# Kernel tuning notes

Measured on AMD Instinct MI355X. Metric: run time of the kernel, lower is better.

## Reference

```python
import jax, jax.numpy as jnp
import numpy as np

BITS = 4
MAXQ = (1 << BITS) - 1          # 15
ELEMS = 32 // BITS              # values packed per int32
GROUPSIZE = 128
M, K, N = 4096, 4096, 11008
G = K // GROUPSIZE              # 32 groups


def dequantize(qweight, scales, qzeros, g_idx):
    """Unpack GPTQ int4 weights -> fp16 [K, N], matching matmul_248_kernel."""
    K_ = g_idx.shape[0]
    N_ = scales.shape[1]
    k = jnp.arange(K_)
    # weight: value k,n packed in qweight[k // ELEMS, n] at bit offset (k % ELEMS)*BITS
    w = (qweight[k // ELEMS] >> ((k % ELEMS) * BITS)[:, None].astype(jnp.int32)) & MAXQ  # [K, N]
    # zeros: value g,n packed in qzeros[g, n // ELEMS] at bit offset (n % ELEMS)*BITS; kernel adds +1
    n = jnp.arange(N_)
    z = ((qzeros[:, n // ELEMS] >> ((n % ELEMS) * BITS)[None, :].astype(jnp.int32)) & MAXQ) + 1  # [G, N]
    gi = g_idx.astype(jnp.int32)
    # b = (b - zeros) * scales, per-group via g_idx row mapping
    W = scales[gi] * (w - z[gi]).astype(scales.dtype)  # fp16 [K, N]
    return W


def setup_inputs() -> dict:
    key = jax.random.key(0)
    k1, k2, k3, k4 = jax.random.split(key, 4)
    x = (jax.random.normal(k1, (M, K), dtype=jnp.float32) * 0.05).astype(jnp.float16)
    imin = jnp.iinfo(jnp.int32).min
    imax = jnp.iinfo(jnp.int32).max
    qweight = jax.random.randint(k2, (K // ELEMS, N), imin, imax, dtype=jnp.int32)
    qzeros = jax.random.randint(k3, (G, N // ELEMS), imin, imax, dtype=jnp.int32)
    scales = (jax.random.uniform(k4, (G, N), dtype=jnp.float32) * 0.009 + 0.001).astype(jnp.float16)
    g_idx = (jnp.arange(K, dtype=jnp.int32) // GROUPSIZE).astype(jnp.int32)
    return {"x": x, "qweight": qweight, "scales": scales, "qzeros": qzeros, "g_idx": g_idx}


def reference(x, qweight, scales, qzeros, g_idx):
    W = dequantize(qweight, scales, qzeros, g_idx)
    # fp16 inputs, fp32 accumulation, fp16 store (as in the Triton kernel)
    out = jnp.dot(x, W, preferred_element_type=jnp.float32).astype(jnp.float16)
    return out
```

## Files before the change

### kernel.cpp

```cpp
#include <hip/hip_runtime.h>

typedef unsigned short u16;
typedef unsigned int   u32;
typedef _Float16       f16;

#define M_DIM 4096
#define K_DIM 4096
#define N_DIM 11008
#define NQ8   (N_DIM / 8)
#define BM 128
#define BN 128
#define BK 32
#define BKP 40

typedef f16   f16x8 __attribute__((ext_vector_type(8)));
typedef f16   f16x2 __attribute__((ext_vector_type(2)));
typedef float f32x4 __attribute__((ext_vector_type(4)));

typedef __attribute__((address_space(1))) void GV;
typedef __attribute__((address_space(3))) void LV;

__device__ __forceinline__ u32 pk2(float lo, float hi) {
    return __builtin_bit_cast(u32, __builtin_amdgcn_cvt_pkrtz(lo, hi));
}

__global__ __launch_bounds__(256) void cvt_x(const float* __restrict__ x, f16* __restrict__ xh) {
    const size_t t = (size_t)blockIdx.x * 256 + threadIdx.x;
    const float4* p = (const float4*)(x + t * 8);
    float4 a0 = p[0], a1 = p[1];
    uint4 v;
    v.x = pk2(a0.x, a1.x); v.y = pk2(a0.y, a1.y);
    v.z = pk2(a0.z, a1.z); v.w = pk2(a0.w, a1.w);
    *(uint4*)(xh + t * 8) = v;
}

template<bool PRE>
__global__ __launch_bounds__(256, 2)
void gptq_gemm(const float* __restrict__ x, const f16* __restrict__ xh,
               const int* __restrict__ qw, const float* __restrict__ sc,
               const int* __restrict__ qz, float* __restrict__ out)
{
    constexpr int AK = PRE ? 32 : 40;
    __shared__ __align__(16) f16 As[BM * AK];
    __shared__ __align__(16) f16 Bs[BN * BKP];

    const int tid  = threadIdx.x;
    const int lane = tid & 63;
    const int wave = tid >> 6;
    const int quad = lane >> 4;
    const int l15  = lane & 15;
    const int wm   = (wave & 1) * 64;
    const int wn   = (wave >> 1) * 64;

    const int m0 = blockIdx.y * BM;
    const int n0 = blockIdx.x * BN;

    const f16* agh0 = xh + (size_t)(m0 + (tid >> 2)) * K_DIM + (tid & 3) * 8;
    const f16* agh1 = agh0 + (size_t)64 * K_DIM;
    f16* al0 = As + tid * 8;
    f16* al1 = As + 2048 + tid * 8;
    const float* agf = x + (size_t)(m0 + (tid >> 1)) * K_DIM + (tid & 1) * 16;
    f16* alf = As + (tid >> 1) * AK + (tid & 1) * 16;

    const int dn  = tid & 127;
    const int dkq = tid >> 7;
    const int gn  = n0 + dn;
    const int zsh = (gn & 7) * 4;
    const int*   qwp = qw + gn;
    const int*   qzp = qz + (gn >> 3);
    const float* scp = sc + gn;
    f16* bs0 = Bs + dn * BKP + dkq * 8;

    f32x4 acc[4][4];
    #pragma unroll
    for (int i = 0; i < 4; i++)
        #pragma unroll
        for (int j = 0; j < 4; j++)
            acc[i][j] = (f32x4){0.f, 0.f, 0.f, 0.f};

    for (int g = 0; g < K_DIM / 128; g++) {
        const u32 zq = (u32)qzp[(size_t)g * NQ8];
        const int z1 = (int)((zq >> zsh) & 15u) + 1;
        const float s = scp[(size_t)g * N_DIM];
        const f16 sh = (f16)s;
        const f16 bh = (f16)(-(float)(1024 + z1));
        const f16x2 s2 = {sh, sh};
        const f16x2 b2 = {bh, bh};

        #pragma unroll
        for (int t = 0; t < 4; t++) {
            const int kt = g * 4 + t;

            if constexpr (PRE) {
                __builtin_amdgcn_global_load_lds((GV*)(agh0 + kt * BK), (LV*)al0, 16, 0, 0);
                __builtin_amdgcn_global_load_lds((GV*)(agh1 + kt * BK), (LV*)al1, 16, 0, 0);
            }

            uint4 bv[2];
            #pragma unroll
            for (int i = 0; i < 2; i++) {
                const u32 q = (u32)qwp[(size_t)(4 * kt + dkq + 2 * i) * N_DIM];
                u32 pk[4];
                #pragma unroll
                for (int j = 0; j < 4; j++) {
                    const u32 mbits = ((q >> (4 * j)) & 0x000F000Fu) | 0x64006400u;
                    f16x2 v2 = __builtin_bit_cast(f16x2, mbits);
                    f16x2 w2 = (v2 + b2) * s2;
                    pk[j] = __builtin_bit_cast(u32, w2);
                }
                bv[i].x = pk[0]; bv[i].y = pk[1]; bv[i].z = pk[2]; bv[i].w = pk[3];
            }

            if constexpr (!PRE) {
                const float4* agp = (const float4*)(agf + kt * BK);
                float4 a0 = agp[0], a1 = agp[1], a2 = agp[2], a3 = agp[3];
                uint4 av0, av1;
                av0.x = pk2(a0.x, a1.x); av0.y = pk2(a0.y, a1.y);
                av0.z = pk2(a0.z, a1.z); av0.w = pk2(a0.w, a1.w);
                av1.x = pk2(a2.x, a3.x); av1.y = pk2(a2.y, a3.y);
                av1.z = pk2(a2.z, a3.z); av1.w = pk2(a2.w, a3.w);
                *(uint4*)(alf)     = av0;
                *(uint4*)(alf + 8) = av1;
            }
            *(uint4*)(bs0)      = bv[0];
            *(uint4*)(bs0 + 16) = bv[1];
            __syncthreads();

            f16x8 af[4], bfr[4];
            #pragma unroll
            for (int t2 = 0; t2 < 4; t2++) {
                af[t2]  = *(const f16x8*)(As + (wm + t2 * 16 + l15) * AK  + quad * 8);
                bfr[t2] = *(const f16x8*)(Bs + (wn + t2 * 16 + l15) * BKP + quad * 8);
            }
            #pragma unroll
            for (int i = 0; i < 4; i++)
                #pragma unroll
                for (int j = 0; j < 4; j++)
                    acc[i][j] = __builtin_amdgcn_mfma_f32_16x16x32_f16(af[i], bfr[j], acc[i][j], 0, 0, 0);
            __syncthreads();
        }
    }

    #pragma unroll
    for (int i = 0; i < 4; i++) {
        const int mrow = m0 + wm + i * 16 + quad * 4;
        #pragma unroll
        for (int j = 0; j < 4; j++) {
            const int ncol = n0 + wn + j * 16 + l15;
            float* op = out + (size_t)mrow * N_DIM + ncol;
            #pragma unroll
            for (int r = 0; r < 4; r++)
                op[(size_t)r * N_DIM] = acc[i][j][r];
        }
    }
}

extern "C" void kernel_launch(void* const* d_in, const int* in_sizes, int n_in,
                              void* d_out, int out_size, void* d_ws, size_t ws_size,
                              hipStream_t stream) {
    const float* x  = (const float*)d_in[0];
    const int*   qw = (const int*)d_in[1];
    const float* sc = (const float*)d_in[2];
    const int*   qz = (const int*)d_in[3];
    float* out = (float*)d_out;
    f16*   xh  = (f16*)d_ws;

    dim3 grid(N_DIM / BN, M_DIM / BM);
    const bool pre = ws_size >= (size_t)M_DIM * K_DIM * sizeof(f16);
    if (pre) {
        cvt_x<<<(M_DIM * K_DIM / 8) / 256, 256, 0, stream>>>(x, xh);
        gptq_gemm<true><<<grid, 256, 0, stream>>>(x, xh, qw, sc, qz, out);
    } else {
        gptq_gemm<false><<<grid, 256, 0, stream>>>(x, xh, qw, sc, qz, out);
    }
}
```

Before: 639.6 us.

## Switch to 32x32x16 MFMA tiles with XOR-swizzled unpadded A LDS layout

```diff
diff --git a/kernel.cpp b/kernel.cpp
--- a/kernel.cpp
+++ b/kernel.cpp
@@ -13,9 +13,9 @@
 #define BK 32
 #define BKP 40
 
-typedef f16   f16x8 __attribute__((ext_vector_type(8)));
-typedef f16   f16x2 __attribute__((ext_vector_type(2)));
-typedef float f32x4 __attribute__((ext_vector_type(4)));
+typedef f16   f16x8  __attribute__((ext_vector_type(8)));
+typedef f16   f16x2  __attribute__((ext_vector_type(2)));
+typedef float f32x16 __attribute__((ext_vector_type(16)));
 
 typedef __attribute__((address_space(1))) void GV;
 typedef __attribute__((address_space(3))) void LV;
@@ -40,27 +40,31 @@
                const int* __restrict__ qw, const float* __restrict__ sc,
                const int* __restrict__ qz, float* __restrict__ out)
 {
-    constexpr int AK = PRE ? 32 : 40;
-    __shared__ __align__(16) f16 As[BM * AK];
+    __shared__ __align__(16) f16 As[BM * BK];
     __shared__ __align__(16) f16 Bs[BN * BKP];
 
     const int tid  = threadIdx.x;
     const int lane = tid & 63;
     const int wave = tid >> 6;
-    const int quad = lane >> 4;
-    const int l15  = lane & 15;
+    const int l31  = lane & 31;
+    const int kb   = lane >> 5;
     const int wm   = (wave & 1) * 64;
     const int wn   = (wave >> 1) * 64;
 
     const int m0 = blockIdx.y * BM;
     const int n0 = blockIdx.x * BN;
 
-    const f16* agh0 = xh + (size_t)(m0 + (tid >> 2)) * K_DIM + (tid & 3) * 8;
+    const int swz = ((tid & 3) ^ ((tid >> 3) & 3)) * 8;
+    const f16* agh0 = xh + (size_t)(m0 + (tid >> 2)) * K_DIM + swz;
     const f16* agh1 = agh0 + (size_t)64 * K_DIM;
     f16* al0 = As + tid * 8;
     f16* al1 = As + 2048 + tid * 8;
-    const float* agf = x + (size_t)(m0 + (tid >> 1)) * K_DIM + (tid & 1) * 16;
-    f16* alf = As + (tid >> 1) * AK + (tid & 1) * 16;
+
+    const int fm   = tid >> 1;
+    const int fh   = tid & 1;
+    const int fsig = (tid >> 2) & 3;
+    const float* agf = x + (size_t)(m0 + fm) * K_DIM;
+    f16* alf = As + fm * BK;
 
     const int dn  = tid & 127;
     const int dkq = tid >> 7;
@@ -71,12 +75,17 @@
     const float* scp = sc + gn;
     f16* bs0 = Bs + dn * BKP + dkq * 8;
 
-    f32x4 acc[4][4];
+    const int sigl = (l31 >> 1) & 3;
+    const f16* pa0 = As + (wm + l31) * BK + ((0 + kb) ^ sigl) * 8;
+    const f16* pa1 = As + (wm + l31) * BK + ((2 + kb) ^ sigl) * 8;
+    const f16* pb  = Bs + (wn + l31) * BKP + kb * 8;
+
+    f32x16 acc[2][2];
     #pragma unroll
-    for (int i = 0; i < 4; i++)
+    for (int i = 0; i < 2; i++)
         #pragma unroll
-        for (int j = 0; j < 4; j++)
-            acc[i][j] = (f32x4){0.f, 0.f, 0.f, 0.f};
+        for (int j = 0; j < 2; j++)
+            acc[i][j] = (f32x16)(0.f);
 
     for (int g = 0; g < K_DIM / 128; g++) {
         const u32 zq = (u32)qzp[(size_t)g * NQ8];
@@ -94,6 +103,17 @@
             if constexpr (PRE) {
                 __builtin_amdgcn_global_load_lds((GV*)(agh0 + kt * BK), (LV*)al0, 16, 0, 0);
                 __builtin_amdgcn_global_load_lds((GV*)(agh1 + kt * BK), (LV*)al1, 16, 0, 0);
+            } else {
+                #pragma unroll
+                for (int e = 0; e < 2; e++) {
+                    const int p = 2 * fh + e;
+                    const float4* src = (const float4*)(agf + kt * BK + ((p ^ fsig) * 8));
+                    float4 a0 = src[0], a1 = src[1];
+                    uint4 v;
+                    v.x = pk2(a0.x, a1.x); v.y = pk2(a0.y, a1.y);
+                    v.z = pk2(a0.z, a1.z); v.w = pk2(a0.w, a1.w);
+                    *(uint4*)(alf + p * 8) = v;
+                }
             }
 
             uint4 bv[2];
@@ -110,49 +130,44 @@
                 }
                 bv[i].x = pk[0]; bv[i].y = pk[1]; bv[i].z = pk[2]; bv[i].w = pk[3];
             }
-
-            if constexpr (!PRE) {
-                const float4* agp = (const float4*)(agf + kt * BK);
-                float4 a0 = agp[0], a1 = agp[1], a2 = agp[2], a3 = agp[3];
-                uint4 av0, av1;
-                av0.x = pk2(a0.x, a1.x); av0.y = pk2(a0.y, a1.y);
-                av0.z = pk2(a0.z, a1.z); av0.w = pk2(a0.w, a1.w);
-                av1.x = pk2(a2.x, a3.x); av1.y = pk2(a2.y, a3.y);
-                av1.z = pk2(a2.z, a3.z); av1.w = pk2(a2.w, a3.w);
-                *(uint4*)(alf)     = av0;
-                *(uint4*)(alf + 8) = av1;
-            }
             *(uint4*)(bs0)      = bv[0];
             *(uint4*)(bs0 + 16) = bv[1];
             __syncthreads();
 
-            f16x8 af[4], bfr[4];
+            f16x8 af[2][2], bf[2][2];
             #pragma unroll
-            for (int t2 = 0; t2 < 4; t2++) {
-                af[t2]  = *(const f16x8*)(As + (wm + t2 * 16 + l15) * AK  + quad * 8);
-                bfr[t2] = *(const f16x8*)(Bs + (wn + t2 * 16 + l15) * BKP + quad * 8);
+            for (int mt = 0; mt < 2; mt++) {
+                af[mt][0] = *(const f16x8*)(pa0 + mt * 32 * BK);
+                af[mt][1] = *(const f16x8*)(pa1 + mt * 32 * BK);
             }
             #pragma unroll
-            for (int i = 0; i < 4; i++)
+            for (int nt = 0; nt < 2; nt++) {
+                bf[nt][0] = *(const f16x8*)(pb + nt * 32 * BKP);
+                bf[nt][1] = *(const f16x8*)(pb + nt * 32 * BKP + 16);
+            }
+            #pragma unroll
+            for (int mt = 0; mt < 2; mt++)
                 #pragma unroll
-                for (int j = 0; j < 4; j++)
-                    acc[i][j] = __builtin_amdgcn_mfma_f32_16x16x32_f16(af[i], bfr[j], acc[i][j], 0, 0, 0);
+                for (int nt = 0; nt < 2; nt++)
+                    #pragma unroll
+                    for (int ks = 0; ks < 2; ks++)
+                        acc[mt][nt] = __builtin_amdgcn_mfma_f32_32x32x16_f16(
+                            af[mt][ks], bf[nt][ks], acc[mt][nt], 0, 0, 0);
             __syncthreads();
         }
     }
 
     #pragma unroll
-    for (int i = 0; i < 4; i++) {
-        const int mrow = m0 + wm + i * 16 + quad * 4;
+    for (int mt = 0; mt < 2; mt++)
         #pragma unroll
-        for (int j = 0; j < 4; j++) {
-            const int ncol = n0 + wn + j * 16 + l15;
-            float* op = out + (size_t)mrow * N_DIM + ncol;
+        for (int nt = 0; nt < 2; nt++) {
+            const int ncol = n0 + wn + nt * 32 + l31;
             #pragma unroll
-            for (int r = 0; r < 4; r++)
-                op[(size_t)r * N_DIM] = acc[i][j][r];
+            for (int r = 0; r < 16; r++) {
+                const int mrow = m0 + wm + mt * 32 + (r & 3) + 8 * (r >> 2) + 4 * kb;
+                out[(size_t)mrow * N_DIM + ncol] = acc[mt][nt][r];
+            }
         }
-    }
 }
 
 extern "C" void kernel_launch(void* const* d_in, const int* in_sizes, int n_in,
```

Result: no change. 643.1 us (+0.6%).
